# Kernel tuning notes

Hardware: AMD Instinct MI355X
Metric: run time of the kernel (lower is better)

The kernel has to match this reference:

```python
import math
import jax, jax.numpy as jnp
import numpy as np

N_HEAD = 16

def skew(QEr):
    # QEr: (B, H, L, L) where last dim indexes relative positions via Er_t
    B, H, L, _ = QEr.shape
    padded = jnp.pad(QEr, ((0, 0), (0, 0), (0, 0), (1, 0)))        # (B,H,L,L+1)
    reshaped = padded.reshape(B, H, L + 1, L)                       # (B,H,L+1,L)
    return reshaped[:, :, 1:, :]                                    # (B,H,L,L)

def setup_inputs() -> dict:
    key = jax.random.key(0)
    ks = jax.random.split(key, 6)
    B, L, D = 2, 2048, 1024
    hs = D // N_HEAD
    block_size = 2048
    return {
        "x": jax.random.normal(ks[0], (B, L, D), dtype=jnp.float32),
        "W_attn": jax.random.normal(ks[1], (D, 3 * D), dtype=jnp.float32) * 0.02,
        "b_attn": jnp.zeros((3 * D,), dtype=jnp.float32),
        "W_proj": jax.random.normal(ks[2], (D, D), dtype=jnp.float32) * 0.02,
        "b_proj": jnp.zeros((D,), dtype=jnp.float32),
        "Er": jax.random.normal(ks[3], (block_size, hs), dtype=jnp.float32),
    }

def reference(x, W_attn, b_attn, W_proj, b_proj, Er):
    B, L, D = x.shape
    H = N_HEAD
    hs = D // H
    qkv = x @ W_attn + b_attn                                       # (B,L,3D)
    q, k, v = jnp.split(qkv, 3, axis=-1)
    q = q.reshape(B, L, H, hs).transpose(0, 2, 1, 3)                # (B,H,L,hs)
    k = k.reshape(B, L, H, hs).transpose(0, 2, 1, 3)
    v = v.reshape(B, L, H, hs).transpose(0, 2, 1, 3)
    start = Er.shape[0] - L
    Er_t = Er[start:, :].T                                          # (hs,L)
    QEr = jnp.einsum('bhld,de->bhle', q, Er_t)                      # (B,H,L,L)
    Srel = skew(QEr)
    QK_t = jnp.einsum('bhqd,bhkd->bhqk', q, k)
    scale = 1.0 / math.sqrt(hs)
    att = (QK_t + Srel) * scale
    causal = jnp.tril(jnp.ones((L, L), dtype=bool))
    att = jnp.where(causal[None, None, :, :], att, -jnp.inf)
    att = jax.nn.softmax(att, axis=-1)
    y = jnp.einsum('bhqk,bhkd->bhqd', att, v)                       # (B,H,L,hs)
    y = y.transpose(0, 2, 1, 3).reshape(B, L, D)
    return y @ W_proj + b_proj
```

## Files before the change

kernel.cpp:

```cpp
#include <hip/hip_runtime.h>
#include <stdint.h>

#define L_SEQ 2048
#define D_MODEL 1024
#define NHEAD 16
#define HS 64
#define B_BATCH 2
#define QSCALE 0.1803368801111243f

typedef __bf16 bf16x8 __attribute__((ext_vector_type(8)));
typedef float f32x4 __attribute__((ext_vector_type(4)));

__device__ __forceinline__ float fexp2(float x) {
  return __builtin_amdgcn_exp2f(x);
}

__device__ __forceinline__ unsigned short f2b(float f) {
  unsigned int u = __float_as_uint(f);
  u += 0x7fffu + ((u >> 16) & 1u);
  return (unsigned short)(u >> 16);
}
__device__ __forceinline__ unsigned int pk2(float a, float b) {
  return (unsigned int)f2b(a) | ((unsigned int)f2b(b) << 16);
}

union U8 { uint4 v; unsigned short s[8]; };

__device__ __forceinline__ void ldsload16(const unsigned short* g, unsigned short* l) {
  __builtin_amdgcn_global_load_lds(
      (const __attribute__((address_space(1))) unsigned int*)g,
      (__attribute__((address_space(3))) unsigned int*)l, 16, 0, 0);
}

__device__ __forceinline__ bf16x8 frag_ld(const unsigned short* base, int row, int ks, int quad) {
  const int unit = (ks * 4 + quad) ^ (row & 7);
  return *(const bf16x8*)(base + row * 64 + unit * 8);
}

__global__ __launch_bounds__(256) void prep(
    const float* __restrict__ x, const float* __restrict__ Wa,
    const float* __restrict__ Wp, const float* __restrict__ Er,
    unsigned short* __restrict__ xb, unsigned short* __restrict__ wabT,
    unsigned short* __restrict__ wpbT, unsigned short* __restrict__ erb) {
  __shared__ unsigned short tt[64][65];
  int gb = blockIdx.x;
  if (gb < 2048) {
    int i = gb * 256 + threadIdx.x;
    const float4* s4 = (const float4*)x;
    float4 a = s4[i * 2], b = s4[i * 2 + 1];
    U8 u;
    u.s[0] = f2b(a.x); u.s[1] = f2b(a.y); u.s[2] = f2b(a.z); u.s[3] = f2b(a.w);
    u.s[4] = f2b(b.x); u.s[5] = f2b(b.y); u.s[6] = f2b(b.z); u.s[7] = f2b(b.w);
    ((uint4*)xb)[i] = u.v;
    return;
  }
  gb -= 2048;
  if (gb < 66) {
    int i = gb * 256 + threadIdx.x;
    if (i < 16384) {
      const float4* s4 = (const float4*)Er;
      float4 a = s4[i * 2], b = s4[i * 2 + 1];
      U8 u;
      u.s[0] = f2b(a.x); u.s[1] = f2b(a.y); u.s[2] = f2b(a.z); u.s[3] = f2b(a.w);
      u.s[4] = f2b(b.x); u.s[5] = f2b(b.y); u.s[6] = f2b(b.z); u.s[7] = f2b(b.w);
      ((uint4*)erb)[i] = u.v;
    } else {
      ((uint4*)erb)[i] = make_uint4(0u, 0u, 0u, 0u);
    }
    return;
  }
  gb -= 66;
  const float* src;
  unsigned short* dst;
  int N, nbx;
  if (gb < 768) { src = Wa; dst = wabT; N = 3072; nbx = 48; }
  else { gb -= 768; src = Wp; dst = wpbT; N = 1024; nbx = 16; }
  const int n0 = (gb % nbx) * 64, k0 = (gb / nbx) * 64;
  const int c = threadIdx.x & 63, r0 = threadIdx.x >> 6;
#pragma unroll
  for (int i = 0; i < 16; i++) {
    int r = r0 * 16 + i;
    tt[r][c] = f2b(src[(size_t)(k0 + r) * N + n0 + c]);
  }
  __syncthreads();
  const int n = threadIdx.x >> 2, ks = (threadIdx.x & 3) * 16;
  U8 u0, u1;
#pragma unroll
  for (int j = 0; j < 8; j++) {
    u0.s[j] = tt[ks + j][n];
    u1.s[j] = tt[ks + 8 + j][n];
  }
  unsigned short* d = dst + (size_t)(n0 + n) * 1024 + k0 + ks;
  *(uint4*)d = u0.v;
  *(uint4*)(d + 8) = u1.v;
}

__global__ __launch_bounds__(256, 3) void gemm_qkv(
    const unsigned short* __restrict__ A, const unsigned short* __restrict__ Bt,
    const float* __restrict__ bias, unsigned short* __restrict__ qbuf,
    unsigned short* __restrict__ kbuf, unsigned short* __restrict__ vbufT,
    int M, int N, int K) {
  __shared__ unsigned short As[128 * 64];
  __shared__ unsigned short Bs[128 * 64];
  const int tid = threadIdx.x, lane = tid & 63, w = tid >> 6;
  const int wm = w >> 1, wn = w & 1, quad = lane >> 4, lc = lane & 15;
  const int bm = blockIdx.y, bn = blockIdx.x;
  const int l8 = lane >> 3, u8 = ((lane & 7) ^ l8) * 8;
  const unsigned short* Ab = A + (size_t)bm * 128 * K;
  const unsigned short* Bb = Bt + (size_t)bn * 128 * K;

  f32x4 z4 = {0.f, 0.f, 0.f, 0.f};
  f32x4 acc[4][4];
#pragma unroll
  for (int mb = 0; mb < 4; mb++)
#pragma unroll
    for (int nb = 0; nb < 4; nb++) acc[mb][nb] = z4;

  for (int kk = 0; kk < K; kk += 64) {
    if (kk) __syncthreads();
#pragma unroll
    for (int i = 0; i < 4; i++) {
      int ch = w * 4 + i;
      ldsload16(Ab + (size_t)(ch * 8 + l8) * K + kk + u8, &As[ch * 512]);
      ldsload16(Bb + (size_t)(ch * 8 + l8) * K + kk + u8, &Bs[ch * 512]);
    }
    __syncthreads();
#pragma unroll
    for (int ks = 0; ks < 2; ks++) {
      bf16x8 af[4], bfv[4];
#pragma unroll
      for (int mb = 0; mb < 4; mb++) af[mb] = frag_ld(As, wm * 64 + mb * 16 + lc, ks, quad);
#pragma unroll
      for (int nb = 0; nb < 4; nb++) bfv[nb] = frag_ld(Bs, wn * 64 + nb * 16 + lc, ks, quad);
#pragma unroll
      for (int mb = 0; mb < 4; mb++)
#pragma unroll
        for (int nb = 0; nb < 4; nb++)
          acc[mb][nb] = __builtin_amdgcn_mfma_f32_16x16x32_bf16(af[mb], bfv[nb],
                                                               acc[mb][nb], 0, 0, 0);
    }
  }

#pragma unroll
  for (int nb = 0; nb < 4; nb++) {
    const int n = bn * 128 + wn * 64 + nb * 16 + lc;
    const float bv = bias[n];
    const int which = n >> 10;
    const int rem = n & 1023;
    const int h = rem >> 6, d = rem & 63;
    const float sc = which == 0 ? QSCALE : 1.0f;
#pragma unroll
    for (int mb = 0; mb < 4; mb++) {
#pragma unroll
      for (int reg = 0; reg < 4; reg++) {
        const int m = bm * 128 + wm * 64 + mb * 16 + quad * 4 + reg;
        const int b = m >> 11, l = m & 2047;
        float val = (acc[mb][nb][reg] + bv) * sc;
        if (which == 0)
          qbuf[((size_t)(b * NHEAD + h) * L_SEQ + l) * HS + d] = f2b(val);
        else if (which == 1)
          kbuf[((size_t)(b * NHEAD + h) * L_SEQ + l) * HS + d] = f2b(val);
        else
          vbufT[((size_t)(b * NHEAD + h) * HS + d) * L_SEQ + l] = f2b(val);
      }
    }
  }
}

__global__ __launch_bounds__(256, 2) void gemm_proj(
    const unsigned short* __restrict__ A, const unsigned short* __restrict__ Bt,
    const float* __restrict__ bias, float* __restrict__ out, int M, int N, int K) {
  __shared__ unsigned short As[128 * 64];
  __shared__ unsigned short Bs[64 * 64];
  const int tid = threadIdx.x, lane = tid & 63, w = tid >> 6;
  const int quad = lane >> 4, lc = lane & 15;
  const int bm = blockIdx.y, bn = blockIdx.x;
  const int l8 = lane >> 3, u8 = ((lane & 7) ^ l8) * 8;
  const unsigned short* Ab = A + (size_t)bm * 128 * K;
  const unsigned short* Bb = Bt + (size_t)bn * 64 * K;

  f32x4 z4 = {0.f, 0.f, 0.f, 0.f};
  f32x4 acc[2][4];
#pragma unroll
  for (int mb = 0; mb < 2; mb++)
#pragma unroll
    for (int nb = 0; nb < 4; nb++) acc[mb][nb] = z4;

  for (int kk = 0; kk < K; kk += 64) {
    if (kk) __syncthreads();
#pragma unroll
    for (int i = 0; i < 4; i++) {
      int ch = w * 4 + i;
      ldsload16(Ab + (size_t)(ch * 8 + l8) * K + kk + u8, &As[ch * 512]);
    }
#pragma unroll
    for (int i = 0; i < 2; i++) {
      int ch = w * 2 + i;
      ldsload16(Bb + (size_t)(ch * 8 + l8) * K + kk + u8, &Bs[ch * 512]);
    }
    __syncthreads();
#pragma unroll
    for (int ks = 0; ks < 2; ks++) {
      bf16x8 af[2], bfv[4];
#pragma unroll
      for (int mb = 0; mb < 2; mb++) af[mb] = frag_ld(As, w * 32 + mb * 16 + lc, ks, quad);
#pragma unroll
      for (int nb = 0; nb < 4; nb++) bfv[nb] = frag_ld(Bs, nb * 16 + lc, ks, quad);
#pragma unroll
      for (int mb = 0; mb < 2; mb++)
#pragma unroll
        for (int nb = 0; nb < 4; nb++)
          acc[mb][nb] = __builtin_amdgcn_mfma_f32_16x16x32_bf16(af[mb], bfv[nb],
                                                               acc[mb][nb], 0, 0, 0);
    }
  }

#pragma unroll
  for (int nb = 0; nb < 4; nb++) {
    const int n = bn * 64 + nb * 16 + lc;
    const float bv = bias[n];
#pragma unroll
    for (int mb = 0; mb < 2; mb++) {
#pragma unroll
      for (int reg = 0; reg < 4; reg++) {
        const int m = bm * 128 + w * 32 + mb * 16 + quad * 4 + reg;
        out[(size_t)m * N + n] = acc[mb][nb][reg] + bv;
      }
    }
  }
}

__global__ __launch_bounds__(256, 3) void flash_attn_rel(
    const unsigned short* __restrict__ qb, const unsigned short* __restrict__ kb,
    const unsigned short* __restrict__ vbT, const unsigned short* __restrict__ erb,
    unsigned short* __restrict__ yb) {
  __shared__ unsigned short Ks[64 * 64];
  __shared__ unsigned short Vt[64 * 64];
  __shared__ unsigned short Es[128 * 64];
  __shared__ float Twf[4][16 * 84];

  const int tid = threadIdx.x, lane = tid & 63, w = tid >> 6;
  const int quad = lane >> 4, lc = lane & 15;
  const int bh = blockIdx.x;
  const int b = bh >> 4, h = bh & 15;
  const int qt = 31 - (int)blockIdx.y;
  const int q0 = qt * 64;
  const int qg0 = q0 + w * 16;
  const size_t hoff = (size_t)bh * L_SEQ * HS;
  float* TwfW = Twf[w];
  unsigned short* TwpW = (unsigned short*)TwfW;
  const int l8 = lane >> 3, u8 = ((lane & 7) ^ l8) * 8;
  const f32x4 z4 = {0.f, 0.f, 0.f, 0.f};

  bf16x8 qf[2];
  {
    const unsigned short* qrow = qb + hoff + (size_t)(qg0 + lc) * HS;
    qf[0] = *(const bf16x8*)(qrow + quad * 8);
    qf[1] = *(const bf16x8*)(qrow + 32 + quad * 8);
  }
  f32x4 Oacc[4];
#pragma unroll
  for (int db = 0; db < 4; db++) Oacc[db] = z4;
  float psum_acc = 0.0f;

  const unsigned short* kgb = kb + hoff;
  const unsigned short* vgbT = vbT + (size_t)bh * HS * L_SEQ;
  const int ebw = 48 - w * 16;

  for (int k0 = 0; k0 <= q0; k0 += 64) {
    __syncthreads();
#pragma unroll
    for (int i = 0; i < 2; i++) {
      int ch = w * 2 + i;
      ldsload16(kgb + (size_t)(k0 + ch * 8 + l8) * HS + u8, &Ks[ch * 512]);
      ldsload16(vgbT + (size_t)(ch * 8 + l8) * L_SEQ + k0 + u8, &Vt[ch * 512]);
    }
    const int e0 = (L_SEQ - 64) - q0 + k0;
#pragma unroll
    for (int i = 0; i < 4; i++) {
      int ch = w * 4 + i;
      ldsload16(erb + (size_t)(e0 + ch * 8 + l8) * HS + u8, &Es[ch * 512]);
    }
    __syncthreads();

    f32x4 sacc[4], tacc[5];
#pragma unroll
    for (int i = 0; i < 4; i++) sacc[i] = z4;
#pragma unroll
    for (int i = 0; i < 5; i++) tacc[i] = z4;
#pragma unroll
    for (int ks = 0; ks < 2; ks++) {
#pragma unroll
      for (int kbi = 0; kbi < 4; kbi++) {
        bf16x8 a = frag_ld(Ks, kbi * 16 + lc, ks, quad);
        sacc[kbi] = __builtin_amdgcn_mfma_f32_16x16x32_bf16(a, qf[ks], sacc[kbi], 0, 0, 0);
      }
#pragma unroll
      for (int eb = 0; eb < 5; eb++) {
        bf16x8 a = frag_ld(Es, ebw + eb * 16 + lc, ks, quad);
        tacc[eb] = __builtin_amdgcn_mfma_f32_16x16x32_bf16(a, qf[ks], tacc[eb], 0, 0, 0);
      }
    }
#pragma unroll
    for (int eb = 0; eb < 5; eb++)
      *(f32x4*)&TwfW[lc * 84 + eb * 16 + quad * 4] = tacc[eb];
    asm volatile("" ::: "memory");

    float p[4][4], ps = 0.0f;
    const int tbase = lc * 84 + (15 - lc);
    if (k0 == q0) {
      const int qrow = w * 16 + lc;
#pragma unroll
      for (int kbi = 0; kbi < 4; kbi++)
#pragma unroll
        for (int reg = 0; reg < 4; reg++) {
          const int kk = kbi * 16 + quad * 4 + reg;
          float t = TwfW[tbase + kk];
          float v = (kk > qrow) ? -1e30f : (sacc[kbi][reg] + t);
          p[kbi][reg] = fexp2(v);
          ps += p[kbi][reg];
        }
    } else {
#pragma unroll
      for (int kbi = 0; kbi < 4; kbi++)
#pragma unroll
        for (int reg = 0; reg < 4; reg++) {
          float t = TwfW[tbase + kbi * 16 + quad * 4 + reg];
          p[kbi][reg] = fexp2(sacc[kbi][reg] + t);
          ps += p[kbi][reg];
        }
    }
    psum_acc += ps;
#pragma unroll
    for (int kbi = 0; kbi < 4; kbi++) {
      uint2 pk;
      pk.x = pk2(p[kbi][0], p[kbi][1]);
      pk.y = pk2(p[kbi][2], p[kbi][3]);
      const int k = kbi * 16 + quad * 4;
      *(uint2*)&TwpW[lc * 64 + (((k >> 3) ^ (lc & 7)) << 3) + (k & 7)] = pk;
    }
    asm volatile("" ::: "memory");

#pragma unroll
    for (int ks = 0; ks < 2; ks++) {
      bf16x8 pf = frag_ld(TwpW, lc, ks, quad);
#pragma unroll
      for (int db = 0; db < 4; db++) {
        bf16x8 av = frag_ld(Vt, db * 16 + lc, ks, quad);
        Oacc[db] = __builtin_amdgcn_mfma_f32_16x16x32_bf16(av, pf, Oacc[db], 0, 0, 0);
      }
    }
  }

  psum_acc += __shfl_xor(psum_acc, 16, 64);
  psum_acc += __shfl_xor(psum_acc, 32, 64);
  const float inv = 1.0f / psum_acc;

  __syncthreads();
  unsigned short* Yt = Es;
#pragma unroll
  for (int db = 0; db < 4; db++) {
    uint2 pk;
    pk.x = pk2(Oacc[db][0] * inv, Oacc[db][1] * inv);
    pk.y = pk2(Oacc[db][2] * inv, Oacc[db][3] * inv);
    *(uint2*)&Yt[(w * 16 + lc) * 72 + db * 16 + quad * 4] = pk;
  }
  __syncthreads();
  {
    const int r = tid >> 2, seg = (tid & 3) * 16;
    uint4 a0 = *(const uint4*)&Yt[r * 72 + seg];
    uint4 a1 = *(const uint4*)&Yt[r * 72 + seg + 8];
    unsigned short* d = yb + (size_t)((size_t)b * L_SEQ + q0 + r) * D_MODEL + h * HS + seg;
    *(uint4*)d = a0;
    *(uint4*)(d + 8) = a1;
  }
}

extern "C" void kernel_launch(void* const* d_in, const int* in_sizes, int n_in,
                              void* d_out, int out_size, void* d_ws, size_t ws_size,
                              hipStream_t stream) {
  const float* x = (const float*)d_in[0];
  const float* W_attn = (const float*)d_in[1];
  const float* b_attn = (const float*)d_in[2];
  const float* W_proj = (const float*)d_in[3];
  const float* b_proj = (const float*)d_in[4];
  const float* Er = (const float*)d_in[5];
  float* out = (float*)d_out;

  const int n_x = B_BATCH * L_SEQ * D_MODEL;
  const int n_wa = D_MODEL * 3 * D_MODEL;
  const int n_wp = D_MODEL * D_MODEL;
  const int n_er_pad = (L_SEQ + 64) * HS;
  const int n_head = B_BATCH * NHEAD * L_SEQ * HS;

  unsigned short* xb = (unsigned short*)d_ws;
  unsigned short* wabT = xb + n_x;
  unsigned short* wpbT = wabT + n_wa;
  unsigned short* erb = wpbT + n_wp;
  unsigned short* qbuf = erb + n_er_pad;
  unsigned short* kbuf = qbuf + n_head;
  unsigned short* vbufT = kbuf + n_head;
  unsigned short* ybuf = vbufT + n_head;

  prep<<<3138, 256, 0, stream>>>(x, W_attn, W_proj, Er, xb, wabT, wpbT, erb);

  gemm_qkv<<<dim3(24, 32), 256, 0, stream>>>(xb, wabT, b_attn, qbuf, kbuf, vbufT,
                                             B_BATCH * L_SEQ, 3 * D_MODEL, D_MODEL);

  flash_attn_rel<<<dim3(B_BATCH * NHEAD, 32), 256, 0, stream>>>(qbuf, kbuf, vbufT,
                                                                erb, ybuf);

  gemm_proj<<<dim3(16, 32), 256, 0, stream>>>(ybuf, wpbT, b_proj, out,
                                              B_BATCH * L_SEQ, D_MODEL, D_MODEL);
}
```

Measured before the change: 201.5 us.

## Split long causal attention rows over key chunks and add reduction kernel

Query tiles with many key blocks are split into up to four 512-key chunks. Each chunk runs as its own workgroup and writes unnormalized fp32 partial outputs and row sums to workspace. A new reduce kernel adds the partials, normalizes them and writes the bf16 output. This evens out the causal triangle's load imbalance and raises the number of workgroups, at the cost of extra fp32 global traffic, one more kernel launch, and a dependence on the workspace being large enough.

```diff
diff --git a/kernel.cpp b/kernel.cpp
--- a/kernel.cpp
+++ b/kernel.cpp
@@ -233,7 +233,8 @@
 __global__ __launch_bounds__(256, 3) void flash_attn_rel(
     const unsigned short* __restrict__ qb, const unsigned short* __restrict__ kb,
     const unsigned short* __restrict__ vbT, const unsigned short* __restrict__ erb,
-    unsigned short* __restrict__ yb) {
+    unsigned short* __restrict__ yb, float* __restrict__ pO,
+    float* __restrict__ ppsum, const int use_split) {
   __shared__ unsigned short Ks[64 * 64];
   __shared__ unsigned short Vt[64 * 64];
   __shared__ unsigned short Es[128 * 64];
@@ -243,8 +244,16 @@
   const int quad = lane >> 4, lc = lane & 15;
   const int bh = blockIdx.x;
   const int b = bh >> 4, h = bh & 15;
-  const int qt = 31 - (int)blockIdx.y;
+  const int y = blockIdx.y;
+  int qt, jc;
+  if (!use_split)      { qt = 31 - y;  jc = 0; }
+  else if (y < 32)     { qt = 31 - y;  jc = 0; }
+  else if (y < 56)     { qt = 63 - y;  jc = 1; }
+  else if (y < 72)     { qt = 87 - y;  jc = 2; }
+  else                 { qt = 103 - y; jc = 3; }
   const int q0 = qt * 64;
+  const int kbeg = use_split ? (jc << 9) : 0;
+  const int kend = use_split ? min(kbeg + 512, q0 + 64) : (q0 + 64);
   const int qg0 = q0 + w * 16;
   const size_t hoff = (size_t)bh * L_SEQ * HS;
   float* TwfW = Twf[w];
@@ -267,7 +276,7 @@
   const unsigned short* vgbT = vbT + (size_t)bh * HS * L_SEQ;
   const int ebw = 48 - w * 16;
 
-  for (int k0 = 0; k0 <= q0; k0 += 64) {
+  for (int k0 = kbeg; k0 < kend; k0 += 64) {
     __syncthreads();
 #pragma unroll
     for (int i = 0; i < 2; i++) {
@@ -354,6 +363,16 @@
 
   psum_acc += __shfl_xor(psum_acc, 16, 64);
   psum_acc += __shfl_xor(psum_acc, 32, 64);
+
+  if (use_split && qt >= 8) {
+    const size_t pbase = ((size_t)bh * 24 + (qt - 8)) * 4 + jc;
+    float* po = pO + pbase * 4096 + (size_t)(w * 16 + lc) * 64 + quad * 4;
+#pragma unroll
+    for (int db = 0; db < 4; db++) *(f32x4*)(po + db * 16) = Oacc[db];
+    if (quad == 0) ppsum[pbase * 64 + w * 16 + lane] = psum_acc;
+    return;
+  }
+
   const float inv = 1.0f / psum_acc;
 
   __syncthreads();
@@ -374,6 +393,45 @@
     *(uint4*)d = a0;
     *(uint4*)(d + 8) = a1;
   }
+}
+
+__global__ __launch_bounds__(256) void flash_reduce(
+    const float* __restrict__ pO, const float* __restrict__ ppsum,
+    unsigned short* __restrict__ yb) {
+  const int bh = blockIdx.x, qy = blockIdx.y;
+  const int qt = qy + 8;
+  const int nch = (qt >> 3) + 1;
+  const int b = bh >> 4, h = bh & 15;
+  const int q0 = qt * 64;
+  const int t = threadIdx.x;
+  const int q = t >> 2, dseg = (t & 3) * 16;
+  const size_t pbase = ((size_t)bh * 24 + qy) * 4;
+  const float* p0 = pO + pbase * 4096 + (size_t)q * 64 + dseg;
+  f32x4 a0 = *(const f32x4*)(p0);
+  f32x4 a1 = *(const f32x4*)(p0 + 4);
+  f32x4 a2 = *(const f32x4*)(p0 + 8);
+  f32x4 a3 = *(const f32x4*)(p0 + 12);
+  float ps = ppsum[pbase * 64 + q];
+  for (int jj = 1; jj < nch; jj++) {
+    const float* pj = p0 + (size_t)jj * 4096;
+    a0 += *(const f32x4*)(pj);
+    a1 += *(const f32x4*)(pj + 4);
+    a2 += *(const f32x4*)(pj + 8);
+    a3 += *(const f32x4*)(pj + 12);
+    ps += ppsum[pbase * 64 + (size_t)jj * 64 + q];
+  }
+  const float inv = 1.0f / ps;
+  U8 u0, u1;
+#pragma unroll
+  for (int i = 0; i < 4; i++) {
+    u0.s[i]     = f2b(a0[i] * inv);
+    u0.s[4 + i] = f2b(a1[i] * inv);
+    u1.s[i]     = f2b(a2[i] * inv);
+    u1.s[4 + i] = f2b(a3[i] * inv);
+  }
+  unsigned short* d = yb + ((size_t)b * L_SEQ + q0 + q) * D_MODEL + h * HS + dseg;
+  *(uint4*)d = u0.v;
+  *(uint4*)(d + 8) = u1.v;
 }
 
 extern "C" void kernel_launch(void* const* d_in, const int* in_sizes, int n_in,
@@ -402,13 +460,24 @@
   unsigned short* vbufT = kbuf + n_head;
   unsigned short* ybuf = vbufT + n_head;
 
+  const size_t n_pO = (size_t)32 * 24 * 4 * 64 * 64;
+  const size_t n_ppsum = (size_t)32 * 24 * 4 * 64;
+  float* pO = (float*)(ybuf + n_x);
+  float* ppsum = pO + n_pO;
+  const size_t base_bytes = ((size_t)ybuf + (size_t)n_x * 2) - (size_t)d_ws;
+  const size_t need = base_bytes + (n_pO + n_ppsum) * sizeof(float);
+  const int use_split = (ws_size >= need) ? 1 : 0;
+
   prep<<<3138, 256, 0, stream>>>(x, W_attn, W_proj, Er, xb, wabT, wpbT, erb);
 
   gemm_qkv<<<dim3(24, 32), 256, 0, stream>>>(xb, wabT, b_attn, qbuf, kbuf, vbufT,
                                              B_BATCH * L_SEQ, 3 * D_MODEL, D_MODEL);
 
-  flash_attn_rel<<<dim3(B_BATCH * NHEAD, 32), 256, 0, stream>>>(qbuf, kbuf, vbufT,
-                                                                erb, ybuf);
+  flash_attn_rel<<<dim3(B_BATCH * NHEAD, use_split ? 80 : 32), 256, 0, stream>>>(
+      qbuf, kbuf, vbufT, erb, ybuf, pO, ppsum, use_split);
+
+  if (use_split)
+    flash_reduce<<<dim3(B_BATCH * NHEAD, 24), 256, 0, stream>>>(pO, ppsum, ybuf);
 
   gemm_proj<<<dim3(16, 32), 256, 0, stream>>>(ybuf, wpbT, b_proj, out,
                                               B_BATCH * L_SEQ, D_MODEL, D_MODEL);
```

Measured after the change: 223.0 us. +10.7%, slower.

## Double query tile per block to 128 rows with ring-buffered Er tile

Applied to the files above, without the earlier changes.

Each attention block now handles 128 query rows (32 per wave, as two 16-row sub-tiles), so every K/V tile loaded into shared memory feeds twice as many MFMAs. The Er window becomes a 256-row ring buffer in LDS: the first iteration loads 192 rows and later iterations load only 64 new rows, and the two sub-tiles share overlapping Er fragments. Grid halves, work is interleaved heavy/light across blockIdx.y, and launch bounds drop to 2 waves per SIMD to fit the larger LDS and register footprint, which lowers occupancy and adds causal-tail imbalance across waves.

```diff
diff --git a/kernel.cpp b/kernel.cpp
--- a/kernel.cpp
+++ b/kernel.cpp
@@ -55,7 +55,7 @@
     return;
   }
   gb -= 2048;
-  if (gb < 66) {
+  if (gb < 68) {
     int i = gb * 256 + threadIdx.x;
     if (i < 16384) {
       const float4* s4 = (const float4*)Er;
@@ -69,7 +69,7 @@
     }
     return;
   }
-  gb -= 66;
+  gb -= 68;
   const float* src;
   unsigned short* dst;
   int N, nbx;
@@ -230,44 +230,50 @@
   }
 }
 
-__global__ __launch_bounds__(256, 3) void flash_attn_rel(
+__global__ __launch_bounds__(256, 2) void flash_attn_rel(
     const unsigned short* __restrict__ qb, const unsigned short* __restrict__ kb,
     const unsigned short* __restrict__ vbT, const unsigned short* __restrict__ erb,
     unsigned short* __restrict__ yb) {
   __shared__ unsigned short Ks[64 * 64];
   __shared__ unsigned short Vt[64 * 64];
-  __shared__ unsigned short Es[128 * 64];
-  __shared__ float Twf[4][16 * 84];
+  __shared__ unsigned short Es[256 * 64];
+  __shared__ float Twf[4][1856];
 
   const int tid = threadIdx.x, lane = tid & 63, w = tid >> 6;
   const int quad = lane >> 4, lc = lane & 15;
   const int bh = blockIdx.x;
   const int b = bh >> 4, h = bh & 15;
-  const int qt = 31 - (int)blockIdx.y;
-  const int q0 = qt * 64;
-  const int qg0 = q0 + w * 16;
+  const int y = (int)blockIdx.y;
+  const int qt = (y < 8) ? (15 - y) : (y - 8);
+  const int q0 = qt * 128;
+  const int qg = q0 + w * 32;
   const size_t hoff = (size_t)bh * L_SEQ * HS;
   float* TwfW = Twf[w];
-  unsigned short* TwpW = (unsigned short*)TwfW;
+  unsigned short* TwpW1 = (unsigned short*)TwfW;
+  unsigned short* TwpW0 = (unsigned short*)(TwfW + 1344);
   const int l8 = lane >> 3, u8 = ((lane & 7) ^ l8) * 8;
   const f32x4 z4 = {0.f, 0.f, 0.f, 0.f};
-
-  bf16x8 qf[2];
-  {
-    const unsigned short* qrow = qb + hoff + (size_t)(qg0 + lc) * HS;
-    qf[0] = *(const bf16x8*)(qrow + quad * 8);
-    qf[1] = *(const bf16x8*)(qrow + 32 + quad * 8);
-  }
-  f32x4 Oacc[4];
-#pragma unroll
-  for (int db = 0; db < 4; db++) Oacc[db] = z4;
-  float psum_acc = 0.0f;
+  const int e_anchor = L_SEQ - 128 - q0;
+
+  bf16x8 qf[2][2];
+#pragma unroll
+  for (int j = 0; j < 2; j++) {
+    const unsigned short* qrow = qb + hoff + (size_t)(qg + j * 16 + lc) * HS;
+    qf[j][0] = *(const bf16x8*)(qrow + quad * 8);
+    qf[j][1] = *(const bf16x8*)(qrow + 32 + quad * 8);
+  }
+  f32x4 Oacc[2][4];
+#pragma unroll
+  for (int j = 0; j < 2; j++)
+#pragma unroll
+    for (int db = 0; db < 4; db++) Oacc[j][db] = z4;
+  float psum[2] = {0.0f, 0.0f};
 
   const unsigned short* kgb = kb + hoff;
   const unsigned short* vgbT = vbT + (size_t)bh * HS * L_SEQ;
-  const int ebw = 48 - w * 16;
-
-  for (int k0 = 0; k0 <= q0; k0 += 64) {
+
+  const int kend = q0 + 128;
+  for (int k0 = 0; k0 < kend; k0 += 64) {
     __syncthreads();
 #pragma unroll
     for (int i = 0; i < 2; i++) {
@@ -275,104 +281,140 @@
       ldsload16(kgb + (size_t)(k0 + ch * 8 + l8) * HS + u8, &Ks[ch * 512]);
       ldsload16(vgbT + (size_t)(ch * 8 + l8) * L_SEQ + k0 + u8, &Vt[ch * 512]);
     }
-    const int e0 = (L_SEQ - 64) - q0 + k0;
-#pragma unroll
-    for (int i = 0; i < 4; i++) {
-      int ch = w * 4 + i;
-      ldsload16(erb + (size_t)(e0 + ch * 8 + l8) * HS + u8, &Es[ch * 512]);
+    if (k0 == 0) {
+#pragma unroll
+      for (int i = 0; i < 6; i++) {
+        int ch = w * 6 + i;
+        ldsload16(erb + (size_t)(e_anchor + ch * 8 + l8) * HS + u8, &Es[ch * 512]);
+      }
+    } else {
+#pragma unroll
+      for (int i = 0; i < 2; i++) {
+        int ch = w * 2 + i;
+        int er = k0 + 128 + ch * 8;
+        ldsload16(erb + (size_t)(e_anchor + er + l8) * HS + u8, &Es[(er & 255) * 64]);
+      }
     }
     __syncthreads();
 
-    f32x4 sacc[4], tacc[5];
-#pragma unroll
-    for (int i = 0; i < 4; i++) sacc[i] = z4;
-#pragma unroll
-    for (int i = 0; i < 5; i++) tacc[i] = z4;
+    if (k0 > qg + 31) continue;
+
+    f32x4 sacc[2][4], tacc[2][5];
+#pragma unroll
+    for (int j = 0; j < 2; j++) {
+#pragma unroll
+      for (int i = 0; i < 4; i++) sacc[j][i] = z4;
+#pragma unroll
+      for (int i = 0; i < 5; i++) tacc[j][i] = z4;
+    }
+    const int ub = 96 - 32 * w + k0;
 #pragma unroll
     for (int ks = 0; ks < 2; ks++) {
 #pragma unroll
       for (int kbi = 0; kbi < 4; kbi++) {
         bf16x8 a = frag_ld(Ks, kbi * 16 + lc, ks, quad);
-        sacc[kbi] = __builtin_amdgcn_mfma_f32_16x16x32_bf16(a, qf[ks], sacc[kbi], 0, 0, 0);
-      }
-#pragma unroll
-      for (int eb = 0; eb < 5; eb++) {
-        bf16x8 a = frag_ld(Es, ebw + eb * 16 + lc, ks, quad);
-        tacc[eb] = __builtin_amdgcn_mfma_f32_16x16x32_bf16(a, qf[ks], tacc[eb], 0, 0, 0);
-      }
-    }
-#pragma unroll
-    for (int eb = 0; eb < 5; eb++)
-      *(f32x4*)&TwfW[lc * 84 + eb * 16 + quad * 4] = tacc[eb];
-    asm volatile("" ::: "memory");
-
-    float p[4][4], ps = 0.0f;
+        sacc[0][kbi] = __builtin_amdgcn_mfma_f32_16x16x32_bf16(a, qf[0][ks], sacc[0][kbi], 0, 0, 0);
+        sacc[1][kbi] = __builtin_amdgcn_mfma_f32_16x16x32_bf16(a, qf[1][ks], sacc[1][kbi], 0, 0, 0);
+      }
+#pragma unroll
+      for (int eb = 0; eb < 6; eb++) {
+        bf16x8 a = frag_ld(Es, (ub + eb * 16 + lc) & 255, ks, quad);
+        if (eb >= 1)
+          tacc[0][eb - 1] = __builtin_amdgcn_mfma_f32_16x16x32_bf16(a, qf[0][ks], tacc[0][eb - 1], 0, 0, 0);
+        if (eb <= 4)
+          tacc[1][eb] = __builtin_amdgcn_mfma_f32_16x16x32_bf16(a, qf[1][ks], tacc[1][eb], 0, 0, 0);
+      }
+    }
+
     const int tbase = lc * 84 + (15 - lc);
-    if (k0 == q0) {
-      const int qrow = w * 16 + lc;
-#pragma unroll
-      for (int kbi = 0; kbi < 4; kbi++)
-#pragma unroll
-        for (int reg = 0; reg < 4; reg++) {
-          const int kk = kbi * 16 + quad * 4 + reg;
-          float t = TwfW[tbase + kk];
-          float v = (kk > qrow) ? -1e30f : (sacc[kbi][reg] + t);
-          p[kbi][reg] = fexp2(v);
-          ps += p[kbi][reg];
-        }
-    } else {
-#pragma unroll
-      for (int kbi = 0; kbi < 4; kbi++)
-#pragma unroll
-        for (int reg = 0; reg < 4; reg++) {
-          float t = TwfW[tbase + kbi * 16 + quad * 4 + reg];
-          p[kbi][reg] = fexp2(sacc[kbi][reg] + t);
-          ps += p[kbi][reg];
-        }
-    }
-    psum_acc += ps;
-#pragma unroll
-    for (int kbi = 0; kbi < 4; kbi++) {
-      uint2 pk;
-      pk.x = pk2(p[kbi][0], p[kbi][1]);
-      pk.y = pk2(p[kbi][2], p[kbi][3]);
-      const int k = kbi * 16 + quad * 4;
-      *(uint2*)&TwpW[lc * 64 + (((k >> 3) ^ (lc & 7)) << 3) + (k & 7)] = pk;
-    }
-    asm volatile("" ::: "memory");
+#pragma unroll
+    for (int j = 0; j < 2; j++) {
+#pragma unroll
+      for (int eb = 0; eb < 5; eb++)
+        *(f32x4*)&TwfW[lc * 84 + eb * 16 + quad * 4] = tacc[j][eb];
+      asm volatile("" ::: "memory");
+
+      float p[4][4], ps = 0.0f;
+      const int qgj = qg + j * 16;
+      if (k0 + 63 > qgj) {
+        const int qrow = qgj + lc;
+#pragma unroll
+        for (int kbi = 0; kbi < 4; kbi++)
+#pragma unroll
+          for (int reg = 0; reg < 4; reg++) {
+            const int kk = kbi * 16 + quad * 4 + reg;
+            float t = TwfW[tbase + kk];
+            float v = (k0 + kk > qrow) ? -1e30f : (sacc[j][kbi][reg] + t);
+            p[kbi][reg] = fexp2(v);
+            ps += p[kbi][reg];
+          }
+      } else {
+#pragma unroll
+        for (int kbi = 0; kbi < 4; kbi++)
+#pragma unroll
+          for (int reg = 0; reg < 4; reg++) {
+            float t = TwfW[tbase + kbi * 16 + quad * 4 + reg];
+            p[kbi][reg] = fexp2(sacc[j][kbi][reg] + t);
+            ps += p[kbi][reg];
+          }
+      }
+      psum[j] += ps;
+      unsigned short* Pdst = j ? TwpW1 : TwpW0;
+#pragma unroll
+      for (int kbi = 0; kbi < 4; kbi++) {
+        uint2 pk;
+        pk.x = pk2(p[kbi][0], p[kbi][1]);
+        pk.y = pk2(p[kbi][2], p[kbi][3]);
+        const int k = kbi * 16 + quad * 4;
+        *(uint2*)&Pdst[lc * 64 + (((k >> 3) ^ (lc & 7)) << 3) + (k & 7)] = pk;
+      }
+      asm volatile("" ::: "memory");
+    }
 
 #pragma unroll
     for (int ks = 0; ks < 2; ks++) {
-      bf16x8 pf = frag_ld(TwpW, lc, ks, quad);
+      bf16x8 pf0 = frag_ld(TwpW0, lc, ks, quad);
+      bf16x8 pf1 = frag_ld(TwpW1, lc, ks, quad);
 #pragma unroll
       for (int db = 0; db < 4; db++) {
         bf16x8 av = frag_ld(Vt, db * 16 + lc, ks, quad);
-        Oacc[db] = __builtin_amdgcn_mfma_f32_16x16x32_bf16(av, pf, Oacc[db], 0, 0, 0);
-      }
-    }
-  }
-
-  psum_acc += __shfl_xor(psum_acc, 16, 64);
-  psum_acc += __shfl_xor(psum_acc, 32, 64);
-  const float inv = 1.0f / psum_acc;
+        Oacc[0][db] = __builtin_amdgcn_mfma_f32_16x16x32_bf16(av, pf0, Oacc[0][db], 0, 0, 0);
+        Oacc[1][db] = __builtin_amdgcn_mfma_f32_16x16x32_bf16(av, pf1, Oacc[1][db], 0, 0, 0);
+      }
+    }
+  }
+
+#pragma unroll
+  for (int j = 0; j < 2; j++) {
+    psum[j] += __shfl_xor(psum[j], 16, 64);
+    psum[j] += __shfl_xor(psum[j], 32, 64);
+  }
 
   __syncthreads();
   unsigned short* Yt = Es;
 #pragma unroll
-  for (int db = 0; db < 4; db++) {
-    uint2 pk;
-    pk.x = pk2(Oacc[db][0] * inv, Oacc[db][1] * inv);
-    pk.y = pk2(Oacc[db][2] * inv, Oacc[db][3] * inv);
-    *(uint2*)&Yt[(w * 16 + lc) * 72 + db * 16 + quad * 4] = pk;
+  for (int j = 0; j < 2; j++) {
+    const float inv = 1.0f / psum[j];
+#pragma unroll
+    for (int db = 0; db < 4; db++) {
+      uint2 pk;
+      pk.x = pk2(Oacc[j][db][0] * inv, Oacc[j][db][1] * inv);
+      pk.y = pk2(Oacc[j][db][2] * inv, Oacc[j][db][3] * inv);
+      *(uint2*)&Yt[(w * 32 + j * 16 + lc) * 72 + db * 16 + quad * 4] = pk;
+    }
   }
   __syncthreads();
   {
-    const int r = tid >> 2, seg = (tid & 3) * 16;
+    const int r = tid >> 1, seg = (tid & 1) * 32;
     uint4 a0 = *(const uint4*)&Yt[r * 72 + seg];
     uint4 a1 = *(const uint4*)&Yt[r * 72 + seg + 8];
+    uint4 a2 = *(const uint4*)&Yt[r * 72 + seg + 16];
+    uint4 a3 = *(const uint4*)&Yt[r * 72 + seg + 24];
     unsigned short* d = yb + (size_t)((size_t)b * L_SEQ + q0 + r) * D_MODEL + h * HS + seg;
     *(uint4*)d = a0;
     *(uint4*)(d + 8) = a1;
+    *(uint4*)(d + 16) = a2;
+    *(uint4*)(d + 24) = a3;
   }
 }
 
@@ -390,7 +432,7 @@
   const int n_x = B_BATCH * L_SEQ * D_MODEL;
   const int n_wa = D_MODEL * 3 * D_MODEL;
   const int n_wp = D_MODEL * D_MODEL;
-  const int n_er_pad = (L_SEQ + 64) * HS;
+  const int n_er_pad = (L_SEQ + 128) * HS;
   const int n_head = B_BATCH * NHEAD * L_SEQ * HS;
 
   unsigned short* xb = (unsigned short*)d_ws;
@@ -402,12 +444,12 @@
   unsigned short* vbufT = kbuf + n_head;
   unsigned short* ybuf = vbufT + n_head;
 
-  prep<<<3138, 256, 0, stream>>>(x, W_attn, W_proj, Er, xb, wabT, wpbT, erb);
+  prep<<<3140, 256, 0, stream>>>(x, W_attn, W_proj, Er, xb, wabT, wpbT, erb);
 
   gemm_qkv<<<dim3(24, 32), 256, 0, stream>>>(xb, wabT, b_attn, qbuf, kbuf, vbufT,
                                              B_BATCH * L_SEQ, 3 * D_MODEL, D_MODEL);
 
-  flash_attn_rel<<<dim3(B_BATCH * NHEAD, 32), 256, 0, stream>>>(qbuf, kbuf, vbufT,
+  flash_attn_rel<<<dim3(B_BATCH * NHEAD, 16), 256, 0, stream>>>(qbuf, kbuf, vbufT,
                                                                 erb, ybuf);
 
   gemm_proj<<<dim3(16, 32), 256, 0, stream>>>(ybuf, wpbT, b_proj, out,
```

Result: slower. 216.7 us (+7.5%).

## Load V and Er fragments directly from global, shrink LDS, raise occupancy

Applied to the files above, without the earlier changes.

The attention kernel stops staging V and the relative-position table Er through shared memory. Each wave now reads its MFMA operands straight from global memory, which cuts LDS to the K tile plus a per-wave scratch area and lets launch bounds request 4 blocks per CU. It also reorders the query-tile schedule to interleave long and short tiles, swaps the software bf16 rounding for the hardware pack-convert instruction, and pads the Er buffer further so the direct reads stay in bounds. The cost is many uncoalesced, latency-exposed global loads inside the inner loop, which the extra occupancy has to hide.

```diff
diff --git a/kernel.cpp b/kernel.cpp
--- a/kernel.cpp
+++ b/kernel.cpp
@@ -22,6 +22,11 @@
 }
 __device__ __forceinline__ unsigned int pk2(float a, float b) {
   return (unsigned int)f2b(a) | ((unsigned int)f2b(b) << 16);
+}
+__device__ __forceinline__ unsigned int cvtpk(float a, float b) {
+  unsigned int r;
+  asm("v_cvt_pk_bf16_f32 %0, %1, %2" : "=v"(r) : "v"(a), "v"(b));
+  return r;
 }
 
 union U8 { uint4 v; unsigned short s[8]; };
@@ -55,7 +60,7 @@
     return;
   }
   gb -= 2048;
-  if (gb < 66) {
+  if (gb < 68) {
     int i = gb * 256 + threadIdx.x;
     if (i < 16384) {
       const float4* s4 = (const float4*)Er;
@@ -69,7 +74,7 @@
     }
     return;
   }
-  gb -= 66;
+  gb -= 68;
   const float* src;
   unsigned short* dst;
   int N, nbx;
@@ -230,20 +235,19 @@
   }
 }
 
-__global__ __launch_bounds__(256, 3) void flash_attn_rel(
+__global__ __launch_bounds__(256, 4) void flash_attn_rel(
     const unsigned short* __restrict__ qb, const unsigned short* __restrict__ kb,
     const unsigned short* __restrict__ vbT, const unsigned short* __restrict__ erb,
     unsigned short* __restrict__ yb) {
   __shared__ unsigned short Ks[64 * 64];
-  __shared__ unsigned short Vt[64 * 64];
-  __shared__ unsigned short Es[128 * 64];
-  __shared__ float Twf[4][16 * 84];
+  __shared__ float Twf[4][1344];
 
   const int tid = threadIdx.x, lane = tid & 63, w = tid >> 6;
   const int quad = lane >> 4, lc = lane & 15;
   const int bh = blockIdx.x;
   const int b = bh >> 4, h = bh & 15;
-  const int qt = 31 - (int)blockIdx.y;
+  const int y = (int)blockIdx.y;
+  const int qt = (y < 16) ? (31 - y) : (y - 16);
   const int q0 = qt * 64;
   const int qg0 = q0 + w * 16;
   const size_t hoff = (size_t)bh * L_SEQ * HS;
@@ -264,8 +268,9 @@
   float psum_acc = 0.0f;
 
   const unsigned short* kgb = kb + hoff;
-  const unsigned short* vgbT = vbT + (size_t)bh * HS * L_SEQ;
-  const int ebw = 48 - w * 16;
+  const unsigned short* vrow = vbT + (size_t)bh * HS * L_SEQ + (size_t)lc * L_SEQ + quad * 8;
+  const unsigned short* erow0 =
+      erb + (size_t)((L_SEQ - 64) - q0 + 48 - 16 * w + lc) * HS + quad * 8;
 
   for (int k0 = 0; k0 <= q0; k0 += 64) {
     __syncthreads();
@@ -273,16 +278,11 @@
     for (int i = 0; i < 2; i++) {
       int ch = w * 2 + i;
       ldsload16(kgb + (size_t)(k0 + ch * 8 + l8) * HS + u8, &Ks[ch * 512]);
-      ldsload16(vgbT + (size_t)(ch * 8 + l8) * L_SEQ + k0 + u8, &Vt[ch * 512]);
-    }
-    const int e0 = (L_SEQ - 64) - q0 + k0;
-#pragma unroll
-    for (int i = 0; i < 4; i++) {
-      int ch = w * 4 + i;
-      ldsload16(erb + (size_t)(e0 + ch * 8 + l8) * HS + u8, &Es[ch * 512]);
     }
     __syncthreads();
 
+    const unsigned short* erow = erow0 + (size_t)k0 * HS;
+
     f32x4 sacc[4], tacc[5];
 #pragma unroll
     for (int i = 0; i < 4; i++) sacc[i] = z4;
@@ -290,16 +290,18 @@
     for (int i = 0; i < 5; i++) tacc[i] = z4;
 #pragma unroll
     for (int ks = 0; ks < 2; ks++) {
+      bf16x8 ef[5];
+#pragma unroll
+      for (int eb = 0; eb < 5; eb++)
+        ef[eb] = *(const bf16x8*)(erow + eb * (16 * HS) + ks * 32);
 #pragma unroll
       for (int kbi = 0; kbi < 4; kbi++) {
         bf16x8 a = frag_ld(Ks, kbi * 16 + lc, ks, quad);
         sacc[kbi] = __builtin_amdgcn_mfma_f32_16x16x32_bf16(a, qf[ks], sacc[kbi], 0, 0, 0);
       }
 #pragma unroll
-      for (int eb = 0; eb < 5; eb++) {
-        bf16x8 a = frag_ld(Es, ebw + eb * 16 + lc, ks, quad);
-        tacc[eb] = __builtin_amdgcn_mfma_f32_16x16x32_bf16(a, qf[ks], tacc[eb], 0, 0, 0);
-      }
+      for (int eb = 0; eb < 5; eb++)
+        tacc[eb] = __builtin_amdgcn_mfma_f32_16x16x32_bf16(ef[eb], qf[ks], tacc[eb], 0, 0, 0);
     }
 #pragma unroll
     for (int eb = 0; eb < 5; eb++)
@@ -334,8 +336,8 @@
 #pragma unroll
     for (int kbi = 0; kbi < 4; kbi++) {
       uint2 pk;
-      pk.x = pk2(p[kbi][0], p[kbi][1]);
-      pk.y = pk2(p[kbi][2], p[kbi][3]);
+      pk.x = cvtpk(p[kbi][0], p[kbi][1]);
+      pk.y = cvtpk(p[kbi][2], p[kbi][3]);
       const int k = kbi * 16 + quad * 4;
       *(uint2*)&TwpW[lc * 64 + (((k >> 3) ^ (lc & 7)) << 3) + (k & 7)] = pk;
     }
@@ -346,7 +348,7 @@
       bf16x8 pf = frag_ld(TwpW, lc, ks, quad);
 #pragma unroll
       for (int db = 0; db < 4; db++) {
-        bf16x8 av = frag_ld(Vt, db * 16 + lc, ks, quad);
+        bf16x8 av = *(const bf16x8*)(vrow + (size_t)db * 16 * L_SEQ + k0 + ks * 32);
         Oacc[db] = __builtin_amdgcn_mfma_f32_16x16x32_bf16(av, pf, Oacc[db], 0, 0, 0);
       }
     }
@@ -357,12 +359,12 @@
   const float inv = 1.0f / psum_acc;
 
   __syncthreads();
-  unsigned short* Yt = Es;
+  unsigned short* Yt = (unsigned short*)&Twf[0][0];
 #pragma unroll
   for (int db = 0; db < 4; db++) {
     uint2 pk;
-    pk.x = pk2(Oacc[db][0] * inv, Oacc[db][1] * inv);
-    pk.y = pk2(Oacc[db][2] * inv, Oacc[db][3] * inv);
+    pk.x = cvtpk(Oacc[db][0] * inv, Oacc[db][1] * inv);
+    pk.y = cvtpk(Oacc[db][2] * inv, Oacc[db][3] * inv);
     *(uint2*)&Yt[(w * 16 + lc) * 72 + db * 16 + quad * 4] = pk;
   }
   __syncthreads();
@@ -390,7 +392,7 @@
   const int n_x = B_BATCH * L_SEQ * D_MODEL;
   const int n_wa = D_MODEL * 3 * D_MODEL;
   const int n_wp = D_MODEL * D_MODEL;
-  const int n_er_pad = (L_SEQ + 64) * HS;
+  const int n_er_pad = (L_SEQ + 128) * HS;
   const int n_head = B_BATCH * NHEAD * L_SEQ * HS;
 
   unsigned short* xb = (unsigned short*)d_ws;
@@ -402,7 +404,7 @@
   unsigned short* vbufT = kbuf + n_head;
   unsigned short* ybuf = vbufT + n_head;
 
-  prep<<<3138, 256, 0, stream>>>(x, W_attn, W_proj, Er, xb, wabT, wpbT, erb);
+  prep<<<3140, 256, 0, stream>>>(x, W_attn, W_proj, Er, xb, wabT, wpbT, erb);
 
   gemm_qkv<<<dim3(24, 32), 256, 0, stream>>>(xb, wabT, b_attn, qbuf, kbuf, vbufT,
                                              B_BATCH * L_SEQ, 3 * D_MODEL, D_MODEL);
```

New measurement: 296.3 us. 1.47x slower.
